# Kernel optimization log

Measured on AMD Instinct MI355X. Metric: run time of the kernel, lower is better.

The kernel has to match this reference:

```python
import jax, jax.numpy as jnp
import numpy as np

P = 512   # pedestrians
E = 32    # embedding_dim
H = 64    # rela hidden dim


def setup_inputs() -> dict:
    key = jax.random.key(0)
    ks = jax.random.split(key, 8)
    return {
        "corr_index": jax.random.normal(ks[0], (P, P, 2), dtype=jnp.float32),
        "rela_ht": jax.random.normal(ks[1], (P, P, H), dtype=jnp.float32),
        "rela_ct": jax.random.normal(ks[2], (P, P, H), dtype=jnp.float32),
        "nei_index": jax.random.randint(ks[3], (P, P), 0, 2, dtype=jnp.int32),
        "W_emb": jax.random.normal(ks[4], (E, 2), dtype=jnp.float32) * 0.3,
        "b_emb": jnp.zeros((E,), dtype=jnp.float32),
        "W_ih": jax.random.normal(ks[5], (4 * H, E), dtype=jnp.float32) * 0.1,
        "W_hh": jax.random.normal(ks[6], (4 * H, H), dtype=jnp.float32) * 0.1,
        "b_ih": jnp.zeros((4 * H,), dtype=jnp.float32),
        "b_hh": jnp.zeros((4 * H,), dtype=jnp.float32),
    }


def reference(corr_index, rela_ht, rela_ct, nei_index, W_emb, b_emb, W_ih, W_hh, b_ih, b_hh):
    ped = corr_index.shape[0]
    hdim = rela_ht.shape[-1]
    # flatten pedestrian pairs: [P*P, ...]
    x = corr_index.reshape(ped * ped, 2)
    h = rela_ht.reshape(ped * ped, hdim)
    c = rela_ct.reshape(ped * ped, hdim)
    mask = (nei_index.reshape(-1) > 0)[:, None]  # [P*P, 1]

    # relative embedding + ReLU (dropout p=0 is identity)
    emb = jax.nn.relu(x @ W_emb.T + b_emb)  # [P*P, E]

    # torch LSTMCell math, gate order i, f, g, o
    gates = emb @ W_ih.T + b_ih + h @ W_hh.T + b_hh  # [P*P, 4H]
    i, f, g, o = jnp.split(gates, 4, axis=-1)
    i = jax.nn.sigmoid(i)
    f = jax.nn.sigmoid(f)
    g = jnp.tanh(g)
    o = jax.nn.sigmoid(o)
    c_new = f * c + i * g
    h_new = o * jnp.tanh(c_new)

    # scatter: only neighbor pairs (mask>0) are updated, others keep old state
    h_out = jnp.where(mask, h_new, h).reshape(ped, ped, hdim)
    c_out = jnp.where(mask, c_new, c).reshape(ped, ped, hdim)
    return h_out, c_out
```

## Files before the change

kernel.cpp:

```cpp
#include <hip/hip_runtime.h>
#include <hip/hip_bf16.h>

#define PED   512
#define HDIM  64
#define EDIM  32
#define NPAIR (PED * PED)
#define GATES 256
#define WF_ELEMS (16 * 64 * 24)
#define OS    68

typedef __attribute__((ext_vector_type(8))) __bf16 bf16x8;
typedef __attribute__((ext_vector_type(4))) float  floatx4;

__device__ __forceinline__ float sigmoidf_fast(float x) {
    return __builtin_amdgcn_rcpf(1.0f + __expf(-x));
}
__device__ __forceinline__ float tanhf_fast(float x) {
    return fmaf(2.0f, __builtin_amdgcn_rcpf(1.0f + __expf(-2.0f * x)), -1.0f);
}

__global__ void sra_prep(const float* __restrict__ W_ih, const float* __restrict__ W_hh,
                         const float* __restrict__ b_ih, const float* __restrict__ b_hh,
                         __bf16* __restrict__ Wf, float* __restrict__ bsum)
{
    int tid = blockIdx.x * 256 + threadIdx.x;
    if (tid < WF_ELEMS) {
        int m    = tid % 24;
        int nl   = tid / 24;
        int lane = nl & 63;
        int nt   = nl >> 6;
        int n = nt * 16 + (lane & 15);
        int k = (m >> 3) * 32 + (lane >> 4) * 8 + (m & 7);
        float w = (k < EDIM) ? W_ih[n * EDIM + k] : W_hh[n * HDIM + (k - EDIM)];
        Wf[tid] = (__bf16)w;
    }
    if (tid < GATES) bsum[tid] = b_ih[tid] + b_hh[tid];
}

__global__ __launch_bounds__(256, 6)
void sra_main(const float* __restrict__ corr,
              const float* __restrict__ ht,
              const float* __restrict__ ct,
              const int*   __restrict__ nei,
              const float* __restrict__ W_emb,
              const float* __restrict__ b_emb,
              const __bf16* __restrict__ Wf,
              const float* __restrict__ bsumg,
              float* __restrict__ h_out,
              float* __restrict__ c_out)
{
    __shared__ float bsum[GATES];
    __shared__ __align__(16) float OT[4][16 * OS];

    const int tid  = threadIdx.x;
    const int wave = tid >> 6;
    const int lane = tid & 63;
    const int lo   = lane & 15;
    const int qu   = lane >> 4;

    bsum[tid] = bsumg[tid];
    __syncthreads();

    float* ot = &OT[wave][0];
    const int tile = blockIdx.x * 4 + wave;
    const int rb   = tile * 16;

    float2 x = *(const float2*)(corr + (size_t)(rb + lo) * 2);
    bf16x8 a0;
#pragma unroll
    for (int j = 0; j < 8; ++j) {
        int e = qu * 8 + j;
        float v = fmaf(x.x, W_emb[e * 2 + 0], fmaf(x.y, W_emb[e * 2 + 1], b_emb[e]));
        a0[j] = (__bf16)fmaxf(v, 0.0f);
    }

    const size_t rowoff = (size_t)(rb + lo) * HDIM + qu * 8;
    float4 h0a = *(const float4*)(ht + rowoff);
    float4 h0b = *(const float4*)(ht + rowoff + 4);
    float4 h1a = *(const float4*)(ht + rowoff + 32);
    float4 h1b = *(const float4*)(ht + rowoff + 36);
    bf16x8 a1, a2;
    a1[0] = (__bf16)h0a.x; a1[1] = (__bf16)h0a.y; a1[2] = (__bf16)h0a.z; a1[3] = (__bf16)h0a.w;
    a1[4] = (__bf16)h0b.x; a1[5] = (__bf16)h0b.y; a1[6] = (__bf16)h0b.z; a1[7] = (__bf16)h0b.w;
    a2[0] = (__bf16)h1a.x; a2[1] = (__bf16)h1a.y; a2[2] = (__bf16)h1a.z; a2[3] = (__bf16)h1a.w;
    a2[4] = (__bf16)h1b.x; a2[5] = (__bf16)h1b.y; a2[6] = (__bf16)h1b.z; a2[7] = (__bf16)h1b.w;

    const __bf16* bbase = Wf + lane * 24;
    const float*  ctb   = ct + (size_t)rb * HDIM;
    const float*  htb   = ht + (size_t)rb * HDIM;

    int msk[4];
#pragma unroll
    for (int r = 0; r < 4; ++r) msk[r] = nei[rb + qu * 4 + r];

    floatx4 hres[4];

#pragma unroll
    for (int tt = 0; tt < 4; ++tt) {
        const __bf16* bpi = bbase + (tt     ) * 1536;
        const __bf16* bpf = bbase + (tt +  4) * 1536;
        const __bf16* bpg = bbase + (tt +  8) * 1536;
        const __bf16* bpo = bbase + (tt + 12) * 1536;

        floatx4 zi = {0.f,0.f,0.f,0.f};
        floatx4 ai = __builtin_amdgcn_mfma_f32_16x16x32_bf16(a0, *(const bf16x8*)(bpi),      zi, 0,0,0);
        floatx4 af = __builtin_amdgcn_mfma_f32_16x16x32_bf16(a0, *(const bf16x8*)(bpf),      zi, 0,0,0);
        floatx4 ag = __builtin_amdgcn_mfma_f32_16x16x32_bf16(a0, *(const bf16x8*)(bpg),      zi, 0,0,0);
        floatx4 ao = __builtin_amdgcn_mfma_f32_16x16x32_bf16(a0, *(const bf16x8*)(bpo),      zi, 0,0,0);
        ai = __builtin_amdgcn_mfma_f32_16x16x32_bf16(a1, *(const bf16x8*)(bpi + 8),  ai, 0,0,0);
        af = __builtin_amdgcn_mfma_f32_16x16x32_bf16(a1, *(const bf16x8*)(bpf + 8),  af, 0,0,0);
        ag = __builtin_amdgcn_mfma_f32_16x16x32_bf16(a1, *(const bf16x8*)(bpg + 8),  ag, 0,0,0);
        ao = __builtin_amdgcn_mfma_f32_16x16x32_bf16(a1, *(const bf16x8*)(bpo + 8),  ao, 0,0,0);
        ai = __builtin_amdgcn_mfma_f32_16x16x32_bf16(a2, *(const bf16x8*)(bpi + 16), ai, 0,0,0);
        af = __builtin_amdgcn_mfma_f32_16x16x32_bf16(a2, *(const bf16x8*)(bpf + 16), af, 0,0,0);
        ag = __builtin_amdgcn_mfma_f32_16x16x32_bf16(a2, *(const bf16x8*)(bpg + 16), ag, 0,0,0);
        ao = __builtin_amdgcn_mfma_f32_16x16x32_bf16(a2, *(const bf16x8*)(bpo + 16), ao, 0,0,0);

        const int k = tt * 16 + lo;
        const float bi  = bsum[k];
        const float bff = bsum[64 + k];
        const float bg  = bsum[128 + k];
        const float bo  = bsum[192 + k];
#pragma unroll
        for (int r = 0; r < 4; ++r) {
            const int rl = qu * 4 + r;
            float cold = ctb[rl * HDIM + k];
            float hold = htb[rl * HDIM + k];
            float iv = sigmoidf_fast(ai[r] + bi);
            float fv = sigmoidf_fast(af[r] + bff);
            float gv = tanhf_fast(ag[r] + bg);
            float ov = sigmoidf_fast(ao[r] + bo);
            float cn = fv * cold + iv * gv;
            float hn = ov * tanhf_fast(cn);
            bool m = msk[r] > 0;
            ot[rl * OS + k] = m ? cn : cold;
            hres[tt][r]     = m ? hn : hold;
        }
    }

    float* hbase = h_out + (size_t)rb * HDIM;
    float* cbase = c_out + (size_t)rb * HDIM;
#pragma unroll
    for (int j = 0; j < 4; ++j) {
        int fi  = j * 64 + lane;
        int row = fi >> 4;
        int c4  = fi & 15;
        float4 vc = *(float4*)(ot + row * OS + c4 * 4);
        *(float4*)(cbase + fi * 4) = vc;
    }

#pragma unroll
    for (int tt = 0; tt < 4; ++tt) {
        const int k = tt * 16 + lo;
#pragma unroll
        for (int r = 0; r < 4; ++r)
            ot[(qu * 4 + r) * OS + k] = hres[tt][r];
    }
#pragma unroll
    for (int j = 0; j < 4; ++j) {
        int fi  = j * 64 + lane;
        int row = fi >> 4;
        int c4  = fi & 15;
        float4 vh = *(float4*)(ot + row * OS + c4 * 4);
        *(float4*)(hbase + fi * 4) = vh;
    }
}

extern "C" void kernel_launch(void* const* d_in, const int* in_sizes, int n_in,
                              void* d_out, int out_size, void* d_ws, size_t ws_size,
                              hipStream_t stream) {
    const float* corr  = (const float*)d_in[0];
    const float* ht    = (const float*)d_in[1];
    const float* ct    = (const float*)d_in[2];
    const int*   nei   = (const int*)  d_in[3];
    const float* W_emb = (const float*)d_in[4];
    const float* b_emb = (const float*)d_in[5];
    const float* W_ih  = (const float*)d_in[6];
    const float* W_hh  = (const float*)d_in[7];
    const float* b_ih  = (const float*)d_in[8];
    const float* b_hh  = (const float*)d_in[9];

    __bf16* Wf   = (__bf16*)d_ws;
    float*  bsum = (float*)((char*)d_ws + WF_ELEMS * 2);

    float* hout = (float*)d_out;
    float* cout = hout + (size_t)NPAIR * HDIM;

    hipLaunchKernelGGL(sra_prep, dim3(96), dim3(256), 0, stream,
                       W_ih, W_hh, b_ih, b_hh, Wf, bsum);
    hipLaunchKernelGGL(sra_main, dim3(NPAIR / 64), dim3(256), 0, stream,
                       corr, ht, ct, nei, W_emb, b_emb, Wf, bsum, hout, cout);
}
```

Measured before the change: 308.0 us.

## Swap MFMA operands so outputs land per-row, drop LDS transpose, stream stores

The MFMA operands are swapped (weights as A, activations as B), so each lane's accumulator holds four consecutive hidden units of one row. Old c/h state and biases can then be read as float4 directly from global memory, and outputs are written as float4 with nontemporal stores. This removes the shared-memory staging buffers, the bias copy and the block barrier. It relies on 16-byte global accesses being strided across rows instead of fully coalesced, and it lowers the launch-bounds occupancy hint from 6 to 4.

```diff
diff --git a/kernel.cpp b/kernel.cpp
--- a/kernel.cpp
+++ b/kernel.cpp
@@ -7,7 +7,6 @@
 #define NPAIR (PED * PED)
 #define GATES 256
 #define WF_ELEMS (16 * 64 * 24)
-#define OS    68
 
 typedef __attribute__((ext_vector_type(8))) __bf16 bf16x8;
 typedef __attribute__((ext_vector_type(4))) float  floatx4;
@@ -17,6 +16,14 @@
 }
 __device__ __forceinline__ float tanhf_fast(float x) {
     return fmaf(2.0f, __builtin_amdgcn_rcpf(1.0f + __expf(-2.0f * x)), -1.0f);
+}
+
+__device__ __forceinline__ void stream_store(float* p, floatx4 v) {
+#if __has_builtin(__builtin_nontemporal_store)
+    __builtin_nontemporal_store(v, (floatx4*)p);
+#else
+    *(floatx4*)p = v;
+#endif
 }
 
 __global__ void sra_prep(const float* __restrict__ W_ih, const float* __restrict__ W_hh,
@@ -37,7 +44,7 @@
     if (tid < GATES) bsum[tid] = b_ih[tid] + b_hh[tid];
 }
 
-__global__ __launch_bounds__(256, 6)
+__global__ __launch_bounds__(256, 4)
 void sra_main(const float* __restrict__ corr,
               const float* __restrict__ ht,
               const float* __restrict__ ct,
@@ -49,120 +56,97 @@
               float* __restrict__ h_out,
               float* __restrict__ c_out)
 {
-    __shared__ float bsum[GATES];
-    __shared__ __align__(16) float OT[4][16 * OS];
-
     const int tid  = threadIdx.x;
-    const int wave = tid >> 6;
     const int lane = tid & 63;
     const int lo   = lane & 15;
     const int qu   = lane >> 4;
 
-    bsum[tid] = bsumg[tid];
-    __syncthreads();
+    const int tile = blockIdx.x * 4 + (tid >> 6);
+    const int row  = tile * 16 + lo;
+    const size_t rowoff = (size_t)row * HDIM;
 
-    float* ot = &OT[wave][0];
-    const int tile = blockIdx.x * 4 + wave;
-    const int rb   = tile * 16;
-
-    float2 x = *(const float2*)(corr + (size_t)(rb + lo) * 2);
-    bf16x8 a0;
+    const float2 xy = *(const float2*)(corr + (size_t)row * 2);
+    bf16x8 b0;
 #pragma unroll
     for (int j = 0; j < 8; ++j) {
-        int e = qu * 8 + j;
-        float v = fmaf(x.x, W_emb[e * 2 + 0], fmaf(x.y, W_emb[e * 2 + 1], b_emb[e]));
-        a0[j] = (__bf16)fmaxf(v, 0.0f);
+        const int e = qu * 8 + j;
+        float v = fmaf(xy.x, W_emb[e * 2 + 0], fmaf(xy.y, W_emb[e * 2 + 1], b_emb[e]));
+        b0[j] = (__bf16)fmaxf(v, 0.0f);
     }
 
-    const size_t rowoff = (size_t)(rb + lo) * HDIM + qu * 8;
-    float4 h0a = *(const float4*)(ht + rowoff);
-    float4 h0b = *(const float4*)(ht + rowoff + 4);
-    float4 h1a = *(const float4*)(ht + rowoff + 32);
-    float4 h1b = *(const float4*)(ht + rowoff + 36);
-    bf16x8 a1, a2;
-    a1[0] = (__bf16)h0a.x; a1[1] = (__bf16)h0a.y; a1[2] = (__bf16)h0a.z; a1[3] = (__bf16)h0a.w;
-    a1[4] = (__bf16)h0b.x; a1[5] = (__bf16)h0b.y; a1[6] = (__bf16)h0b.z; a1[7] = (__bf16)h0b.w;
-    a2[0] = (__bf16)h1a.x; a2[1] = (__bf16)h1a.y; a2[2] = (__bf16)h1a.z; a2[3] = (__bf16)h1a.w;
-    a2[4] = (__bf16)h1b.x; a2[5] = (__bf16)h1b.y; a2[6] = (__bf16)h1b.z; a2[7] = (__bf16)h1b.w;
+    const floatx4 h0a = *(const floatx4*)(ht + rowoff + qu * 8);
+    const floatx4 h0b = *(const floatx4*)(ht + rowoff + qu * 8 + 4);
+    const floatx4 h1a = *(const floatx4*)(ht + rowoff + 32 + qu * 8);
+    const floatx4 h1b = *(const floatx4*)(ht + rowoff + 32 + qu * 8 + 4);
+    bf16x8 b1, b2;
+#pragma unroll
+    for (int j = 0; j < 4; ++j) {
+        b1[j]     = (__bf16)h0a[j];
+        b1[j + 4] = (__bf16)h0b[j];
+        b2[j]     = (__bf16)h1a[j];
+        b2[j + 4] = (__bf16)h1b[j];
+    }
 
+    const bool msk = nei[row] > 0;
     const __bf16* bbase = Wf + lane * 24;
-    const float*  ctb   = ct + (size_t)rb * HDIM;
-    const float*  htb   = ht + (size_t)rb * HDIM;
-
-    int msk[4];
-#pragma unroll
-    for (int r = 0; r < 4; ++r) msk[r] = nei[rb + qu * 4 + r];
-
-    floatx4 hres[4];
 
 #pragma unroll
-    for (int tt = 0; tt < 4; ++tt) {
-        const __bf16* bpi = bbase + (tt     ) * 1536;
-        const __bf16* bpf = bbase + (tt +  4) * 1536;
-        const __bf16* bpg = bbase + (tt +  8) * 1536;
-        const __bf16* bpo = bbase + (tt + 12) * 1536;
+    for (int g = 0; g < 4; ++g) {
+        const int kb = g * 16 + qu * 4;
 
-        floatx4 zi = {0.f,0.f,0.f,0.f};
-        floatx4 ai = __builtin_amdgcn_mfma_f32_16x16x32_bf16(a0, *(const bf16x8*)(bpi),      zi, 0,0,0);
-        floatx4 af = __builtin_amdgcn_mfma_f32_16x16x32_bf16(a0, *(const bf16x8*)(bpf),      zi, 0,0,0);
-        floatx4 ag = __builtin_amdgcn_mfma_f32_16x16x32_bf16(a0, *(const bf16x8*)(bpg),      zi, 0,0,0);
-        floatx4 ao = __builtin_amdgcn_mfma_f32_16x16x32_bf16(a0, *(const bf16x8*)(bpo),      zi, 0,0,0);
-        ai = __builtin_amdgcn_mfma_f32_16x16x32_bf16(a1, *(const bf16x8*)(bpi + 8),  ai, 0,0,0);
-        af = __builtin_amdgcn_mfma_f32_16x16x32_bf16(a1, *(const bf16x8*)(bpf + 8),  af, 0,0,0);
-        ag = __builtin_amdgcn_mfma_f32_16x16x32_bf16(a1, *(const bf16x8*)(bpg + 8),  ag, 0,0,0);
-        ao = __builtin_amdgcn_mfma_f32_16x16x32_bf16(a1, *(const bf16x8*)(bpo + 8),  ao, 0,0,0);
-        ai = __builtin_amdgcn_mfma_f32_16x16x32_bf16(a2, *(const bf16x8*)(bpi + 16), ai, 0,0,0);
-        af = __builtin_amdgcn_mfma_f32_16x16x32_bf16(a2, *(const bf16x8*)(bpf + 16), af, 0,0,0);
-        ag = __builtin_amdgcn_mfma_f32_16x16x32_bf16(a2, *(const bf16x8*)(bpg + 16), ag, 0,0,0);
-        ao = __builtin_amdgcn_mfma_f32_16x16x32_bf16(a2, *(const bf16x8*)(bpo + 16), ao, 0,0,0);
+        const floatx4 cold = *(const floatx4*)(ct + rowoff + kb);
+        const floatx4 hold = *(const floatx4*)(ht + rowoff + kb);
+        const floatx4 bi4  = *(const floatx4*)(bsumg + kb);
+        const floatx4 bf4  = *(const floatx4*)(bsumg + 64 + kb);
+        const floatx4 bg4  = *(const floatx4*)(bsumg + 128 + kb);
+        const floatx4 bo4  = *(const floatx4*)(bsumg + 192 + kb);
 
-        const int k = tt * 16 + lo;
-        const float bi  = bsum[k];
-        const float bff = bsum[64 + k];
-        const float bg  = bsum[128 + k];
-        const float bo  = bsum[192 + k];
+        const __bf16* pi = bbase + (g     ) * 1536;
+        const __bf16* pf = bbase + (g +  4) * 1536;
+        const __bf16* pg = bbase + (g +  8) * 1536;
+        const __bf16* po = bbase + (g + 12) * 1536;
+
+        const bf16x8 wi0 = *(const bf16x8*)(pi);
+        const bf16x8 wi1 = *(const bf16x8*)(pi + 8);
+        const bf16x8 wi2 = *(const bf16x8*)(pi + 16);
+        const bf16x8 wf0 = *(const bf16x8*)(pf);
+        const bf16x8 wf1 = *(const bf16x8*)(pf + 8);
+        const bf16x8 wf2 = *(const bf16x8*)(pf + 16);
+        const bf16x8 wg0 = *(const bf16x8*)(pg);
+        const bf16x8 wg1 = *(const bf16x8*)(pg + 8);
+        const bf16x8 wg2 = *(const bf16x8*)(pg + 16);
+        const bf16x8 wo0 = *(const bf16x8*)(po);
+        const bf16x8 wo1 = *(const bf16x8*)(po + 8);
+        const bf16x8 wo2 = *(const bf16x8*)(po + 16);
+
+        const floatx4 z = {0.f, 0.f, 0.f, 0.f};
+        floatx4 ai = __builtin_amdgcn_mfma_f32_16x16x32_bf16(wi0, b0, z, 0, 0, 0);
+        floatx4 af = __builtin_amdgcn_mfma_f32_16x16x32_bf16(wf0, b0, z, 0, 0, 0);
+        floatx4 ag = __builtin_amdgcn_mfma_f32_16x16x32_bf16(wg0, b0, z, 0, 0, 0);
+        floatx4 ao = __builtin_amdgcn_mfma_f32_16x16x32_bf16(wo0, b0, z, 0, 0, 0);
+        ai = __builtin_amdgcn_mfma_f32_16x16x32_bf16(wi1, b1, ai, 0, 0, 0);
+        af = __builtin_amdgcn_mfma_f32_16x16x32_bf16(wf1, b1, af, 0, 0, 0);
+        ag = __builtin_amdgcn_mfma_f32_16x16x32_bf16(wg1, b1, ag, 0, 0, 0);
+        ao = __builtin_amdgcn_mfma_f32_16x16x32_bf16(wo1, b1, ao, 0, 0, 0);
+        ai = __builtin_amdgcn_mfma_f32_16x16x32_bf16(wi2, b2, ai, 0, 0, 0);
+        af = __builtin_amdgcn_mfma_f32_16x16x32_bf16(wf2, b2, af, 0, 0, 0);
+        ag = __builtin_amdgcn_mfma_f32_16x16x32_bf16(wg2, b2, ag, 0, 0, 0);
+        ao = __builtin_amdgcn_mfma_f32_16x16x32_bf16(wo2, b2, ao, 0, 0, 0);
+
+        floatx4 cn4, hn4;
 #pragma unroll
         for (int r = 0; r < 4; ++r) {
-            const int rl = qu * 4 + r;
-            float cold = ctb[rl * HDIM + k];
-            float hold = htb[rl * HDIM + k];
-            float iv = sigmoidf_fast(ai[r] + bi);
-            float fv = sigmoidf_fast(af[r] + bff);
-            float gv = tanhf_fast(ag[r] + bg);
-            float ov = sigmoidf_fast(ao[r] + bo);
-            float cn = fv * cold + iv * gv;
-            float hn = ov * tanhf_fast(cn);
-            bool m = msk[r] > 0;
-            ot[rl * OS + k] = m ? cn : cold;
-            hres[tt][r]     = m ? hn : hold;
+            const float iv = sigmoidf_fast(ai[r] + bi4[r]);
+            const float fv = sigmoidf_fast(af[r] + bf4[r]);
+            const float gv = tanhf_fast(ag[r] + bg4[r]);
+            const float ov = sigmoidf_fast(ao[r] + bo4[r]);
+            const float cn = fv * cold[r] + iv * gv;
+            const float hn = ov * tanhf_fast(cn);
+            cn4[r] = msk ? cn : cold[r];
+            hn4[r] = msk ? hn : hold[r];
         }
-    }
-
-    float* hbase = h_out + (size_t)rb * HDIM;
-    float* cbase = c_out + (size_t)rb * HDIM;
-#pragma unroll
-    for (int j = 0; j < 4; ++j) {
-        int fi  = j * 64 + lane;
-        int row = fi >> 4;
-        int c4  = fi & 15;
-        float4 vc = *(float4*)(ot + row * OS + c4 * 4);
-        *(float4*)(cbase + fi * 4) = vc;
-    }
-
-#pragma unroll
-    for (int tt = 0; tt < 4; ++tt) {
-        const int k = tt * 16 + lo;
-#pragma unroll
-        for (int r = 0; r < 4; ++r)
-            ot[(qu * 4 + r) * OS + k] = hres[tt][r];
-    }
-#pragma unroll
-    for (int j = 0; j < 4; ++j) {
-        int fi  = j * 64 + lane;
-        int row = fi >> 4;
-        int c4  = fi & 15;
-        float4 vh = *(float4*)(ot + row * OS + c4 * 4);
-        *(float4*)(hbase + fi * 4) = vh;
+        stream_store(c_out + rowoff + kb, cn4);
+        stream_store(h_out + rowoff + kb, hn4);
     }
 }
 
```

New measurement: 330.5 us. 1.07x slower.
